# Kernel optimization log

Hardware: AMD Instinct MI355X
Metric: run time of the kernel (lower is better)

Reference implementation:

```python
import jax, jax.numpy as jnp
import numpy as np
from jax import lax

B, NQ, C = 2, 1024, 2048
H, DH = 16, 128
G, CD = 4, 512          # off_grps, off_dim = C // G
LR, HR = 24, 72         # low-res grid side, high-res grid side
INTER = 64
K = LR * LR             # sampled K/V tokens (grid_size == lr_size)


def setup_inputs() -> dict:
    key = jax.random.key(0)
    ks = jax.random.split(key, 16)
    s = 0.02
    d = {}
    d['hidden_states'] = jax.random.normal(ks[0], (B, NQ, C), jnp.float32)
    d['image_hd'] = jax.random.normal(ks[1], (B, HR * HR, C), jnp.float32)
    d['wq'] = jax.random.normal(ks[2], (C, C), jnp.float32) * s
    d['wk'] = jax.random.normal(ks[3], (C, C), jnp.float32) * s
    d['wv'] = jax.random.normal(ks[4], (C, C), jnp.float32) * s
    d['wo'] = jax.random.normal(ks[5], (C, C), jnp.float32) * s
    d['conv_dw_w'] = jax.random.normal(ks[6], (CD, 1, 3, 3), jnp.float32) * s
    d['ln1_w'] = jnp.ones((CD,), jnp.float32)
    d['ln1_b'] = jnp.zeros((CD,), jnp.float32)
    d['conv_lr_proj_w'] = jax.random.normal(ks[7], (INTER, CD), jnp.float32) * s
    d['proj_int_w'] = jax.random.normal(ks[8], (INTER, CD), jnp.float32) * s
    d['proj_int_b'] = jnp.zeros((INTER,), jnp.float32)
    d['ln2_w'] = jnp.ones((INTER,), jnp.float32)
    d['ln2_b'] = jnp.zeros((INTER,), jnp.float32)
    d['conv_off_w'] = jax.random.normal(ks[9], (2, INTER), jnp.float32) * s
    d['k_hd_w'] = jax.random.normal(ks[10], (C, C), jnp.float32) * s
    d['k_hd_b'] = jnp.zeros((C,), jnp.float32)
    d['v_hd_w'] = jax.random.normal(ks[11], (C, C), jnp.float32) * s
    d['v_hd_b'] = jnp.zeros((C,), jnp.float32)
    return d


def _ln_channels(x, w, b, eps=1e-5):
    # LayerNorm2d: normalize over channel axis of [N, C, H, W]
    mu = jnp.mean(x, axis=1, keepdims=True)
    var = jnp.var(x, axis=1, keepdims=True)
    xn = (x - mu) * lax.rsqrt(var + eps)
    return xn * w[None, :, None, None] + b[None, :, None, None]


def _tokens_to_grid(x, S):
    # [B, S*S, C] -> [B*G, CD, S, S]  (group channels like einops '(b) (h w) (g c) -> (b g) c h w')
    return x.reshape(B, S, S, G, CD).transpose(0, 3, 4, 1, 2).reshape(B * G, CD, S, S)


def _bilinear_sample(img, grid):
    # img [N, C, Hh, Wh]; grid [N, K, 2] (x, y) normalized to [-1, 1], align_corners=True
    N, Cc, Hh, Wh = img.shape
    x = (grid[..., 0] + 1.0) * 0.5 * (Wh - 1)
    y = (grid[..., 1] + 1.0) * 0.5 * (Hh - 1)
    x0f, y0f = jnp.floor(x), jnp.floor(y)
    wx = (x - x0f)[:, None, :]
    wy = (y - y0f)[:, None, :]
    x0 = jnp.clip(x0f.astype(jnp.int32), 0, Wh - 1)
    x1 = jnp.clip(x0 + 1, 0, Wh - 1)
    y0 = jnp.clip(y0f.astype(jnp.int32), 0, Hh - 1)
    y1 = jnp.clip(y0 + 1, 0, Hh - 1)
    imgf = img.reshape(N, Cc, Hh * Wh)
    gather = jax.vmap(lambda im, ix: im[:, ix])  # ([C,HW],[K]) -> [C,K]
    v00 = gather(imgf, y0 * Wh + x0)
    v01 = gather(imgf, y0 * Wh + x1)
    v10 = gather(imgf, y1 * Wh + x0)
    v11 = gather(imgf, y1 * Wh + x1)
    return (v00 * (1 - wx) * (1 - wy) + v01 * wx * (1 - wy)
            + v10 * (1 - wx) * wy + v11 * wx * wy)  # [N, C, K]


def _ref_grid():
    # normalized reference points as in _grid_generate (centers / (S-1) * 2 - 1)
    yy = (jnp.linspace(0.5, LR - 0.5, LR) / (LR - 1.0)) * 2.0 - 1.0
    xx = (jnp.linspace(0.5, LR - 0.5, LR) / (LR - 1.0)) * 2.0 - 1.0
    gy, gx = jnp.meshgrid(yy, xx, indexing='ij')
    return jnp.stack([gx, gy], axis=-1).reshape(K, 2)  # (x, y)


def reference(hidden_states, image_hd, wq, wk, wv, wo, conv_dw_w, ln1_w, ln1_b,
              conv_lr_proj_w, proj_int_w, proj_int_b, ln2_w, ln2_b, conv_off_w,
              k_hd_w, k_hd_b, v_hd_w, v_hd_b):
    # ---- QKV on the full sequence ----
    q = hidden_states @ wq.T
    k_txt = hidden_states @ wk.T
    v_txt = hidden_states @ wv.T

    # ---- offset network on LR image tokens (first LR*LR tokens) ----
    lr = _tokens_to_grid(hidden_states[:, :K, :], LR)          # [B*G, CD, LR, LR]
    x = lax.conv_general_dilated(lr, conv_dw_w, (1, 1), 'SAME',
                                 feature_group_count=CD,
                                 dimension_numbers=('NCHW', 'OIHW', 'NCHW'))
    x = jax.nn.silu(x)
    x = _ln_channels(x, ln1_w, ln1_b)
    x = jnp.einsum('nchw,oc->nohw', x, conv_lr_proj_w)          # 1x1 conv -> [B*G, INTER, LR, LR]
    # intention gate from spatially pooled group features
    pooled = jnp.mean(lr, axis=(2, 3))                          # [B*G, CD]
    gate = jax.nn.sigmoid(pooled @ proj_int_w.T + proj_int_b)   # [B*G, INTER]
    x = x * gate[:, :, None, None]
    x = _ln_channels(x, ln2_w, ln2_b)
    off = jnp.einsum('nchw,oc->nohw', x, conv_off_w)            # [B*G, 2, LR, LR]
    off = off.transpose(0, 2, 3, 1).reshape(B * G, K, 2)        # (x, y)
    pos = jnp.tanh(_ref_grid()[None] + off)                     # sampling locs in [-1, 1]

    # ---- deformable gather from HD features ----
    hd = _tokens_to_grid(image_hd, HR)                          # [B*G, CD, HR, HR]
    samp = _bilinear_sample(hd, pos)                            # [B*G, CD, K]
    samp = samp.reshape(B, G, CD, K).transpose(0, 3, 1, 2).reshape(B, K, C)
    k_hd = samp @ k_hd_w.T + k_hd_b
    v_hd = samp @ v_hd_w.T + v_hd_b

    # ---- attention: causal over text tokens, HD tokens fully visible ----
    k_all = jnp.concatenate([k_txt, k_hd], axis=1)              # [B, NQ+K, C]
    v_all = jnp.concatenate([v_txt, v_hd], axis=1)
    qh = q.reshape(B, NQ, H, DH).transpose(0, 2, 1, 3)
    kh = k_all.reshape(B, NQ + K, H, DH).transpose(0, 2, 1, 3)
    vh = v_all.reshape(B, NQ + K, H, DH).transpose(0, 2, 1, 3)
    scores = jnp.einsum('bhqd,bhkd->bhqk', qh, kh) / jnp.sqrt(jnp.float32(DH))
    col = jnp.arange(NQ + K)
    row = jnp.arange(NQ)
    allow = (col[None, :] >= NQ) | (col[None, :] <= row[:, None])
    scores = jnp.where(allow[None, None], scores, jnp.float32(-1e9))
    attn = jax.nn.softmax(scores, axis=-1)
    out = jnp.einsum('bhqk,bhkd->bhqd', attn, vh)
    out = out.transpose(0, 2, 1, 3).reshape(B, NQ, C)
    return out @ wo.T
```

## Files before the change

kernel.cpp:

```cpp
#include <hip/hip_runtime.h>

typedef unsigned short u16;
typedef unsigned int u32;
typedef __attribute__((ext_vector_type(8))) short bf8;
typedef __attribute__((ext_vector_type(4))) float f4;
typedef __attribute__((ext_vector_type(4))) unsigned short us4;

constexpr int B = 2;
constexpr int NQ = 1024;
constexpr int C = 2048;
constexpr int DH = 128;
constexpr int G = 4;
constexpr int CD = 512;
constexpr int LR = 24;
constexpr int HR = 72;
constexpr int INTER = 64;
constexpr int K = LR * LR;
constexpr int NKV = NQ + K;

#define MFMA16(a, b, c) __builtin_amdgcn_mfma_f32_16x16x32_bf16(a, b, c, 0, 0, 0)
#define GLDS(g, l)                                                         \
  __builtin_amdgcn_global_load_lds(                                        \
      (const __attribute__((address_space(1))) void*)(g),                  \
      (__attribute__((address_space(3))) void*)(l), 16, 0, 0)
#define SB()                               \
  do {                                     \
    __builtin_amdgcn_sched_barrier(0);     \
    __builtin_amdgcn_s_barrier();          \
    __builtin_amdgcn_sched_barrier(0);     \
  } while (0)
#define WVM(n)                                              \
  do {                                                      \
    asm volatile("s_waitcnt vmcnt(" #n ")" ::: "memory");   \
    __builtin_amdgcn_sched_barrier(0);                      \
  } while (0)

__device__ __forceinline__ u16 f2bf1(float f) {
  u32 u = __float_as_uint(f);
  u32 r = (u + 0x7fffu + ((u >> 16) & 1u)) >> 16;
  return (u16)r;
}

__global__ __launch_bounds__(256) void f2bf_k9(
    const float* __restrict__ s0, const float* __restrict__ s1,
    const float* __restrict__ s2, const float* __restrict__ s3,
    const float* __restrict__ s4, const float* __restrict__ s5,
    const float* __restrict__ s6, const float* __restrict__ plrw,
    const float* __restrict__ cdw, u16* __restrict__ d0, u16* __restrict__ d1,
    u16* __restrict__ d2, u16* __restrict__ d3, u16* __restrict__ d4,
    u16* __restrict__ d5, u16* __restrict__ d6, float* __restrict__ wt,
    float* __restrict__ x1, float* __restrict__ pooled) {
  __shared__ float SH[32 * 577];
  const int y = blockIdx.y;
  const int t = threadIdx.x;
  if (y == 7) {
    if (blockIdx.x >= 128) return;
    const int idx = blockIdx.x * 256 + t;
    wt[idx] = plrw[(idx & 63) * 512 + (idx >> 6)];
    return;
  }
  if (y == 8) {
    if (blockIdx.x >= 128) return;
    const int n = blockIdx.x >> 4, cg = blockIdx.x & 15;
    const int b = n >> 2, g = n & 3;
    const int c0 = cg * 32;
    {
      const int c = t & 31, pr = t >> 5;
      const float* src = s0 + (size_t)b * 1024 * 2048 + g * 512 + c0 + c;
#pragma unroll 4
      for (int j = 0; j < 72; ++j) {
        const int p = j * 8 + pr;
        SH[c * 577 + p] = src[(size_t)p * 2048];
      }
    }
    __syncthreads();
    {
      const int c = t >> 3, seg = t & 7;
      float s = 0.f;
      for (int i = 0; i < 72; ++i) s += SH[c * 577 + seg * 72 + i];
      s += __shfl_xor(s, 1);
      s += __shfl_xor(s, 2);
      s += __shfl_xor(s, 4);
      if (seg == 0) pooled[n * 512 + c0 + c] = s * (1.f / 576.f);
    }
    const size_t base_out = (size_t)(n * 512 + c0) * 576;
    for (int j = 0; j < 72; ++j) {
      const int idx = j * 256 + t;
      const int c = idx / 576, p = idx - c * 576;
      const int yy0 = p / 24, xx0 = p - yy0 * 24;
      const float* wp = cdw + (c0 + c) * 9;
      float s = 0.f;
#pragma unroll
      for (int dy = -1; dy <= 1; ++dy)
#pragma unroll
        for (int dx = -1; dx <= 1; ++dx) {
          const int yy = yy0 + dy, xx = xx0 + dx;
          if (yy < 0 || yy >= 24 || xx < 0 || xx >= 24) continue;
          s += SH[c * 577 + yy * 24 + xx] * wp[(dy + 1) * 3 + dx + 1];
        }
      x1[base_out + idx] = s / (1.f + expf(-s));
    }
    return;
  }
  const float* s;
  u16* d;
  switch (y) {
    case 0: s = s0; d = d0; break;
    case 1: s = s1; d = d1; break;
    case 2: s = s2; d = d2; break;
    case 3: s = s3; d = d3; break;
    case 4: s = s4; d = d4; break;
    case 5: s = s5; d = d5; break;
    default: s = s6; d = d6; break;
  }
  u16* L = (u16*)SH;
  const int pc = blockIdx.x;
  const int mb = pc >> 5, kb = pc & 31;
  const int rin = t >> 2, c0 = (t & 3) * 16;
  const float* src = s + (size_t)(mb * 64 + rin) * 2048 + kb * 64 + c0;
#pragma unroll
  for (int j = 0; j < 16; j += 4) {
    float4 v = *(const float4*)(src + j);
    L[rin * 68 + c0 + j] = f2bf1(v.x);
    L[rin * 68 + c0 + j + 1] = f2bf1(v.y);
    L[rin * 68 + c0 + j + 2] = f2bf1(v.z);
    L[rin * 68 + c0 + j + 3] = f2bf1(v.w);
  }
  __syncthreads();
  u16* dst = d + (size_t)pc * 4096 + t * 16;
#pragma unroll
  for (int gg = 0; gg < 2; ++gg) {
    const int g = t * 2 + gg;
    const int rh = g & 15, ks2 = (g >> 4) & 3, kc = (g >> 6) & 1, fr = g >> 7;
    const int row = fr * 16 + rh, cc = kc * 32 + ks2 * 8;
    us4 o0, o1;
    o0.x = L[row * 68 + cc];     o0.y = L[row * 68 + cc + 1];
    o0.z = L[row * 68 + cc + 2]; o0.w = L[row * 68 + cc + 3];
    o1.x = L[row * 68 + cc + 4]; o1.y = L[row * 68 + cc + 5];
    o1.z = L[row * 68 + cc + 6]; o1.w = L[row * 68 + cc + 7];
    *(us4*)(dst + gg * 8) = o0;
    *(us4*)(dst + gg * 8 + 4) = o1;
  }
}

__global__ __launch_bounds__(512, 2) void gemm256(
    const u16* __restrict__ Ast, const u16* __restrict__ Wq,
    const u16* __restrict__ Wk, const u16* __restrict__ Wv,
    u16* __restrict__ outq, u16* __restrict__ kg, u16* __restrict__ vg) {
  __shared__ u16 As[2][4][4096];
  __shared__ u16 Bs[2][4][4096];
  const int tid = threadIdx.x, lane = tid & 63, w = tid >> 6;
  const int ks = lane >> 4, r = lane & 15;
  const int bid = blockIdx.x;
  const int wm = w >> 2, wn = w & 3;
  const int swz = (bid & 7) * 24 + (bid >> 3);
  const int mt = swz / 24, nt = swz % 24;
  const u16* Wst = (nt < 8) ? Wq : (nt < 16) ? Wk : Wv;
  const int nb0 = (nt & 7) * 4;
  const int mb0 = mt * 4;

#define ST_A03(bi, kt)                                                        \
  do {                                                                        \
    GLDS(Ast + ((size_t)(mb0 + 0) * 32 + (kt)) * 4096 + tid * 8,              \
         &As[bi][0][tid * 8]);                                                \
    GLDS(Ast + ((size_t)(mb0 + 2) * 32 + (kt)) * 4096 + tid * 8,              \
         &As[bi][2][tid * 8]);                                                \
  } while (0)
#define ST_A47(bi, kt)                                                        \
  do {                                                                        \
    GLDS(Ast + ((size_t)(mb0 + 1) * 32 + (kt)) * 4096 + tid * 8,              \
         &As[bi][1][tid * 8]);                                                \
    GLDS(Ast + ((size_t)(mb0 + 3) * 32 + (kt)) * 4096 + tid * 8,              \
         &As[bi][3][tid * 8]);                                                \
  } while (0)
#define ST_B01(bi, kt)                                                        \
  do {                                                                        \
    GLDS(Wst + ((size_t)(nb0 + 0) * 32 + (kt)) * 4096 + tid * 8,              \
         &Bs[bi][0][tid * 8]);                                                \
    GLDS(Wst + ((size_t)(nb0 + 1) * 32 + (kt)) * 4096 + tid * 8,              \
         &Bs[bi][1][tid * 8]);                                                \
  } while (0)
#define ST_B23(bi, kt)                                                        \
  do {                                                                        \
    GLDS(Wst + ((size_t)(nb0 + 2) * 32 + (kt)) * 4096 + tid * 8,              \
         &Bs[bi][2][tid * 8]);                                                \
    GLDS(Wst + ((size_t)(nb0 + 3) * 32 + (kt)) * 4096 + tid * 8,              \
         &Bs[bi][3][tid * 8]);                                                \
  } while (0)
#define RD_A(dst, bi, half, kc)                                               \
  _Pragma("unroll") for (int i2 = 0; i2 < 4; ++i2) dst[i2] =                  \
      *(const bf8*)(&As[bi][wm * 2 + (half)]                                  \
                       [((i2 * 2 + (kc)) * 4 + ks) * 128 + r * 8]);
#define RD_B(dst, bi, kc)                                                     \
  _Pragma("unroll") for (int j2 = 0; j2 < 4; ++j2) dst[j2] =                  \
      *(const bf8*)(&Bs[bi][wn][((j2 * 2 + (kc)) * 4 + ks) * 128 + r * 8]);
#define MM(ACC, AF, BF)                                                       \
  do {                                                                        \
    __builtin_amdgcn_s_setprio(1);                                            \
    _Pragma("unroll") for (int i3 = 0; i3 < 4; ++i3)                          \
        _Pragma("unroll") for (int j3 = 0; j3 < 4; ++j3) ACC[i3][j3] =        \
            MFMA16(AF[i3], BF[j3], ACC[i3][j3]);                              \
    __builtin_amdgcn_s_setprio(0);                                            \
  } while (0)

  f4 accA[4][4], accB[4][4];
#pragma unroll
  for (int i = 0; i < 4; ++i)
#pragma unroll
    for (int j = 0; j < 4; ++j) {
      accA[i][j] = f4{0.f, 0.f, 0.f, 0.f};
      accB[i][j] = f4{0.f, 0.f, 0.f, 0.f};
    }
  bf8 af[4], b0[4], b1[4];

  ST_A03(0, 0); ST_B01(0, 0); ST_B23(0, 0); ST_A47(0, 0);
  ST_A03(1, 1); ST_B01(1, 1);
  WVM(6);
  SB();

  for (int t = 0; t < 32; ++t) {
    const int buf = t & 1;
    RD_A(af, buf, 0, 0);
    RD_B(b0, buf, 0);
    if (t + 1 < 32) ST_B23(buf ^ 1, t + 1);
    SB();
    MM(accA, af, b0);
    SB();
    RD_A(af, buf, 0, 1);
    RD_B(b1, buf, 1);
    if (t + 1 < 32) ST_A47(buf ^ 1, t + 1);
    SB();
    MM(accA, af, b1);
    if (t + 1 < 32) { WVM(8); } else { WVM(0); }
    SB();
    RD_A(af, buf, 1, 0);
    if (t + 2 < 32) ST_A03(buf, t + 2);
    SB();
    MM(accB, af, b0);
    SB();
    RD_A(af, buf, 1, 1);
    if (t + 2 < 32) ST_B01(buf, t + 2);
    SB();
    MM(accB, af, b1);
    if (t + 2 < 32) { WVM(6); } else if (t + 1 < 32) { WVM(2); }
    SB();
  }

#define EPI(ACC, HALF)                                                        \
  _Pragma("unroll") for (int i = 0; i < 4; ++i)                               \
      _Pragma("unroll") for (int j = 0; j < 4; ++j)                           \
          _Pragma("unroll") for (int rr = 0; rr < 4; ++rr) {                  \
    const int m = mt * 256 + wm * 128 + (HALF)*64 + i * 16 + ks * 4 + rr;     \
    const int n = nt * 256 + wn * 64 + j * 16 + r;                            \
    const float v = ACC[i][j][rr];                                            \
    const int sel = n >> 11, nn = n & 2047, hh = nn >> 7, dd = nn & 127;      \
    const int bb = m >> 10, qq = m & 1023;                                    \
    const u16 bv = f2bf1(v);                                                  \
    if (sel == 0) {                                                           \
      outq[(size_t)m * 2048 + nn] = bv;                                       \
    } else if (sel == 1) {                                                    \
      kg[(((size_t)(bb * 16 + hh) * 50 + (qq >> 5)) * 16 + (dd >> 3)) * 256 + \
         (qq & 31) * 8 + (dd & 7)] = bv;                                      \
    } else {                                                                  \
      vg[((size_t)(bb * 16 + hh) * 200 + (qq >> 3)) * 1024 + dd * 8 +         \
         (qq & 7)] = bv;                                                      \
    }                                                                         \
  }
  EPI(accA, 0)
  EPI(accB, 1)
#undef EPI
}

template <int MODE>
__global__ __launch_bounds__(256) void gemm_ho(
    const u16* __restrict__ Ast, const u16* __restrict__ W0,
    const u16* __restrict__ W1, const float* __restrict__ khb,
    const float* __restrict__ vhb, u16* __restrict__ kg,
    u16* __restrict__ vg, float* __restrict__ outf) {
  __shared__ u16 As[3][4096];
  __shared__ u16 Bs[3][4096];
  const int tid = threadIdx.x, lane = tid & 63, w = tid >> 6;
  const int wr = w >> 1, wc = w & 1;
  const int ksl = lane >> 4, rl = lane & 15;
  int mt, nt;
  const u16* Wp;
  if (MODE == 0) {
    const int xcd = blockIdx.x & 7, idx = blockIdx.x >> 3;
    mt = idx >> 2;
    nt = xcd * 4 + (idx & 3);
    Wp = (nt < 16) ? W0 : W1;
  } else {
    const int xcd = blockIdx.x & 7, idx = blockIdx.x >> 3;
    mt = (xcd >> 2) * 8 + idx / 4;
    nt = (xcd & 3) * 4 + idx % 4;
    Wp = W0;
  }
  const int ma0 = mt * 2;
  const int nb0 = (nt & 15) * 2;

#define GST2(dstArr, srcBase, tb0, kt)                                     \
  do {                                                                     \
    const int kb_ = (kt) >> 1, kc_ = (kt) & 1;                             \
    _Pragma("unroll") for (int r2 = 0; r2 < 2; ++r2) {                     \
      const int run = r2 * 4 + w;                                          \
      GLDS(srcBase + ((size_t)((tb0) + (run >> 2)) * 32 + kb_) * 4096 +    \
               (run & 3) * 1024 + kc_ * 512 + lane * 8,                    \
           &dstArr[run * 512 + lane * 8]);                                 \
    }                                                                      \
  } while (0)

  f4 acc[4][4];
#pragma unroll
  for (int i = 0; i < 4; ++i)
#pragma unroll
    for (int j = 0; j < 4; ++j) acc[i][j] = f4{0.f, 0.f, 0.f, 0.f};

  GST2(As[0], Ast, ma0, 0);
  GST2(Bs[0], Wp, nb0, 0);
  GST2(As[1], Ast, ma0, 1);
  GST2(Bs[1], Wp, nb0, 1);
  int rd = 0;
  for (int kt = 0; kt < 64; ++kt) {
    SB();
    if (kt + 2 < 64) {
      const int wb = (rd + 2 >= 3) ? rd - 1 : rd + 2;
      GST2(As[wb], Ast, ma0, kt + 2);
      GST2(Bs[wb], Wp, nb0, kt + 2);
      WVM(8);
    } else if (kt + 1 < 64) {
      WVM(4);
    } else {
      WVM(0);
    }
    SB();
    bf8 af[4], bw[4];
#pragma unroll
    for (int i = 0; i < 4; ++i)
      af[i] = *(const bf8*)(&As[rd][(wr * 4 + i) * 512 + ksl * 128 + rl * 8]);
#pragma unroll
    for (int j = 0; j < 4; ++j)
      bw[j] = *(const bf8*)(&Bs[rd][(wc * 4 + j) * 512 + ksl * 128 + rl * 8]);
    __builtin_amdgcn_s_setprio(1);
#pragma unroll
    for (int i = 0; i < 4; ++i)
#pragma unroll
      for (int j = 0; j < 4; ++j)
        acc[i][j] = MFMA16(af[i], bw[j], acc[i][j]);
    __builtin_amdgcn_s_setprio(0);
    rd = (rd + 1 >= 3) ? 0 : rd + 1;
  }
#undef GST2

  const int rbase = ksl * 4;
  if (MODE == 1) {
#pragma unroll
    for (int i = 0; i < 4; ++i)
#pragma unroll
      for (int j = 0; j < 4; ++j) {
        const int n = nt * 128 + wc * 64 + j * 16 + rl;
#pragma unroll
        for (int rr = 0; rr < 4; ++rr) {
          const int m = mt * 128 + wr * 64 + i * 16 + rbase + rr;
          outf[(size_t)m * 2048 + n] = acc[i][j][rr];
        }
      }
  } else {
    const bool is_v = (nt >= 16);
    const float* bias = is_v ? vhb : khb;
#pragma unroll
    for (int i = 0; i < 4; ++i)
#pragma unroll
      for (int j = 0; j < 4; ++j) {
        const int nn = (nt & 15) * 128 + wc * 64 + j * 16 + rl;
        const int hh = nn >> 7, dd = nn & 127;
#pragma unroll
        for (int rr = 0; rr < 4; ++rr) {
          const int m = mt * 128 + wr * 64 + i * 16 + rbase + rr;
          const int bb = m / 576;
          const int kv = 1024 + (m - bb * 576);
          const u16 bv = f2bf1(acc[i][j][rr] + bias[nn]);
          if (!is_v) {
            kg[(((size_t)(bb * 16 + hh) * 50 + (kv >> 5)) * 16 + (dd >> 3)) *
                   256 +
               (kv & 31) * 8 + (dd & 7)] = bv;
          } else {
            vg[((size_t)(bb * 16 + hh) * 200 + (kv >> 3)) * 1024 + dd * 8 +
               (kv & 7)] = bv;
          }
        }
      }
  }
}

__global__ __launch_bounds__(256) void lnproj_gate(
    const float* __restrict__ x1, const float* __restrict__ ln1w,
    const float* __restrict__ ln1b, const float* __restrict__ wt,
    const float* __restrict__ pooled, const float* __restrict__ piw,
    const float* __restrict__ pib, float* __restrict__ x2,
    float* __restrict__ gate) {
  __shared__ float Xs[512][68];
  __shared__ float rs[4][64], rss[4][64];
  const int bidx = blockIdx.x;
  const int t = threadIdx.x;
  if (bidx >= 72) {
    const int idx = (bidx - 72) * 256 + t;
    const int n = idx >> 6, o = idx & 63;
    const float* pb = pooled + n * 512;
    const float* wb = piw + o * 512;
    float s = pib[o];
    for (int c = 0; c < 512; ++c) s += pb[c] * wb[c];
    gate[idx] = 1.f / (1.f + expf(-s));
    return;
  }
  const int n = bidx / 9, pc = bidx % 9;
  const int p0 = pc * 64;
  {
    const int pl = t & 63, c4 = t >> 6;
    const float* src = x1 + (size_t)n * 512 * 576 + p0 + pl;
#pragma unroll 4
    for (int j = 0; j < 128; ++j) {
      const int c = j * 4 + c4;
      Xs[c][pl] = src[(size_t)c * 576];
    }
  }
  __syncthreads();
  {
    const int pl = t & 63, q = t >> 6;
    float s = 0.f, ss = 0.f;
    for (int c = q * 128; c < q * 128 + 128; ++c) {
      const float v = Xs[c][pl];
      s += v;
      ss += v * v;
    }
    rs[q][pl] = s;
    rss[q][pl] = ss;
    __syncthreads();
    const float S = rs[0][pl] + rs[1][pl] + rs[2][pl] + rs[3][pl];
    const float SS = rss[0][pl] + rss[1][pl] + rss[2][pl] + rss[3][pl];
    const float mean = S * (1.f / 512.f);
    const float inv = rsqrtf(SS * (1.f / 512.f) - mean * mean + 1e-5f);
    for (int c = q * 128; c < q * 128 + 128; ++c)
      Xs[c][pl] = (Xs[c][pl] - mean) * inv * ln1w[c] + ln1b[c];
  }
  __syncthreads();
  {
    const int o4 = (t & 15) * 4, pl0 = (t >> 4) * 4;
    float acc[4][4] = {};
    for (int c = 0; c < 512; ++c) {
      const f4 xv = *(const f4*)(&Xs[c][pl0]);
      const f4 wv = *(const f4*)(&wt[c * 64 + o4]);
#pragma unroll
      for (int i = 0; i < 4; ++i)
#pragma unroll
        for (int j = 0; j < 4; ++j) acc[i][j] += wv[i] * xv[j];
    }
#pragma unroll
    for (int i = 0; i < 4; ++i) {
      f4 ov;
      ov[0] = acc[i][0]; ov[1] = acc[i][1];
      ov[2] = acc[i][2]; ov[3] = acc[i][3];
      *(f4*)(&x2[(size_t)(n * 64 + o4 + i) * 576 + p0 + pl0]) = ov;
    }
  }
}

__global__ __launch_bounds__(256) void pos_sample(
    const float* __restrict__ x2, const float* __restrict__ gate,
    const float* __restrict__ ln2w, const float* __restrict__ ln2b,
    const float* __restrict__ offw, const float* __restrict__ img,
    u16* __restrict__ sampst) {
  const int bk = blockIdx.x;
  const int b = bk / K, k = bk % K;
  __shared__ int s_idx[G][4];
  __shared__ float s_w[G][4];
  const int t = threadIdx.x;
  const int g = t >> 6, lane = t & 63;
  {
    const int n = b * G + g;
    float v = x2[((size_t)n * INTER + lane) * K + k] * gate[n * INTER + lane];
    float s = v, ss = v * v;
    for (int o = 32; o; o >>= 1) {
      s += __shfl_xor(s, o);
      ss += __shfl_xor(ss, o);
    }
    const float mean = s * (1.f / INTER);
    const float var = ss * (1.f / INTER) - mean * mean;
    const float xn = (v - mean) * rsqrtf(var + 1e-5f) * ln2w[lane] + ln2b[lane];
    float ox = xn * offw[lane];
    float oy = xn * offw[INTER + lane];
    for (int o = 32; o; o >>= 1) {
      ox += __shfl_xor(ox, o);
      oy += __shfl_xor(oy, o);
    }
    if (lane == 0) {
      const int yi = k / LR, xi = k % LR;
      const float rx = (xi + 0.5f) / 23.f * 2.f - 1.f;
      const float ry = (yi + 0.5f) / 23.f * 2.f - 1.f;
      const float px = tanhf(rx + ox), py = tanhf(ry + oy);
      const float x = (px + 1.f) * 0.5f * (HR - 1);
      const float y = (py + 1.f) * 0.5f * (HR - 1);
      const float x0f = floorf(x), y0f = floorf(y);
      const float wx = x - x0f, wy = y - y0f;
      const int x0 = min(max((int)x0f, 0), HR - 1);
      const int x1 = min(x0 + 1, HR - 1);
      const int y0 = min(max((int)y0f, 0), HR - 1);
      const int y1 = min(y0 + 1, HR - 1);
      s_idx[g][0] = y0 * HR + x0;
      s_idx[g][1] = y0 * HR + x1;
      s_idx[g][2] = y1 * HR + x0;
      s_idx[g][3] = y1 * HR + x1;
      s_w[g][0] = (1.f - wx) * (1.f - wy);
      s_w[g][1] = wx * (1.f - wy);
      s_w[g][2] = (1.f - wx) * wy;
      s_w[g][3] = wx * wy;
    }
  }
  __syncthreads();
  const int m = b * 576 + k;
  const int mb = m >> 6, fr = (m >> 4) & 3, r = m & 15;
  const int ch0 = t * 8;
  const int gg = ch0 >> 9;
  const float* ib = img + (size_t)b * HR * HR * C + ch0;
  float v[8];
#pragma unroll
  for (int j = 0; j < 8; ++j) v[j] = 0.f;
#pragma unroll
  for (int q = 0; q < 4; ++q) {
    const float wq_ = s_w[gg][q];
    const float* p = ib + (size_t)s_idx[gg][q] * C;
    const float4 a = *(const float4*)p;
    const float4 c = *(const float4*)(p + 4);
    v[0] += wq_ * a.x; v[1] += wq_ * a.y; v[2] += wq_ * a.z; v[3] += wq_ * a.w;
    v[4] += wq_ * c.x; v[5] += wq_ * c.y; v[6] += wq_ * c.z; v[7] += wq_ * c.w;
  }
  const int kb = ch0 >> 6, kc = (ch0 >> 5) & 1, ks3 = (ch0 >> 3) & 3;
  u16* dst = sampst + ((size_t)(mb * 32 + kb)) * 4096 +
             (((fr * 2 + kc) * 4 + ks3) * 16 + r) * 8;
  us4 o0, o1;
  o0.x = f2bf1(v[0]); o0.y = f2bf1(v[1]); o0.z = f2bf1(v[2]); o0.w = f2bf1(v[3]);
  o1.x = f2bf1(v[4]); o1.y = f2bf1(v[5]); o1.z = f2bf1(v[6]); o1.w = f2bf1(v[7]);
  *(us4*)dst = o0;
  *(us4*)(dst + 4) = o1;
}

__global__ __launch_bounds__(256) void attn_u(
    const u16* __restrict__ qb, const u16* __restrict__ kg,
    const u16* __restrict__ vg, u16* __restrict__ aob_st) {
  const int i = blockIdx.x;
  const int pair = i & 255, half = i >> 8;
  const int bh = pair & 31;
  const int q8 = pair >> 5;
  const int qblk = half ? (15 - q8) : q8;
  const int b = bh >> 4, h = bh & 15;
  const int q0 = qblk * 64;
  const int tid = threadIdx.x, lane = tid & 63, w = tid >> 6;
  const int qw = q0 + w * 16;
  const int col = lane & 15, kpart = lane >> 4, rbase = kpart * 4;
  __shared__ u16 Ks[2][4096];
  __shared__ u16 Vs[2][4096];
  __shared__ u16 Pl[4][16 * 40];
  bf8 qf[4];
  {
    const u16* qp =
        qb + (size_t)(b * 1024 + qw + col) * 2048 + h * 128 + kpart * 8;
#pragma unroll
    for (int dc = 0; dc < 4; ++dc) qf[dc] = *(const bf8*)(qp + dc * 32);
  }
  f4 o[8];
#pragma unroll
  for (int df = 0; df < 8; ++df) o[df] = f4{0.f, 0.f, 0.f, 0.f};
  float m_r[4] = {-1e30f, -1e30f, -1e30f, -1e30f};
  float l_p[4] = {0.f, 0.f, 0.f, 0.f};
  const float scale = 0.08838834764831845f;
  const int nt_text = (q0 + 64) >> 5;
  const int nt = nt_text + 18;
  const u16* kbh = kg + (size_t)bh * (NKV * 128);
  const u16* vbh = vg + (size_t)bh * (NKV * 128);
  u16* pw = &Pl[w][0];

#define ASTAGE(bi, kv0)                                                       \
  do {                                                                        \
    const u16* gk = kbh + (size_t)((kv0) >> 5) * 4096 + w * 1024 + lane * 8;  \
    GLDS(gk, &Ks[bi][w * 1024 + lane * 8]);                                   \
    GLDS(gk + 512, &Ks[bi][w * 1024 + 512 + lane * 8]);                       \
    const u16* gv = vbh + (size_t)((kv0) >> 3) * 1024 + w * 1024 + lane * 8;  \
    GLDS(gv, &Vs[bi][w * 1024 + lane * 8]);                                   \
    GLDS(gv + 512, &Vs[bi][w * 1024 + 512 + lane * 8]);                       \
  } while (0)

  ASTAGE(0, 0);
  int cur = 0;
  for (int t = 0; t < nt; ++t) {
    const bool is_text = t < nt_text;
    const int kv0 = is_text ? (t << 5) : (1024 + ((t - nt_text) << 5));
    SB();
    if (t + 1 < nt) {
      const int t1 = t + 1;
      const int kv1 =
          (t1 < nt_text) ? (t1 << 5) : (1024 + ((t1 - nt_text) << 5));
      ASTAGE(cur ^ 1, kv1);
      WVM(4);
    } else {
      WVM(0);
    }
    SB();
    const u16* ksb = &Ks[cur][0];
    const u16* vsb = &Vs[cur][0];
    f4 s0 = {0.f, 0.f, 0.f, 0.f}, s1 = {0.f, 0.f, 0.f, 0.f};
    __builtin_amdgcn_s_setprio(1);
#pragma unroll
    for (int dc = 0; dc < 4; ++dc) {
      const int dblk = dc * 4 + kpart;
      bf8 k0f = *(const bf8*)(ksb + (dblk * 32 + col) * 8);
      bf8 k1f = *(const bf8*)(ksb + (dblk * 32 + 16 + col) * 8);
      s0 = MFMA16(qf[dc], k0f, s0);
      s1 = MFMA16(qf[dc], k1f, s1);
    }
    __builtin_amdgcn_s_setprio(0);
    float sa[4], sc[4], loc[4], p0[4], p1[4];
    bool grow = false;
    const bool need_mask = is_text && (kv0 + 31 > qw);
#pragma unroll
    for (int rr = 0; rr < 4; ++rr) {
      float a = s0[rr] * scale, c2 = s1[rr] * scale;
      if (need_mask) {
        const int qg = qw + rbase + rr;
        if (kv0 + col > qg) a = -1e30f;
        if (kv0 + 16 + col > qg) c2 = -1e30f;
      }
      sa[rr] = a; sc[rr] = c2;
      loc[rr] = fmaxf(a, c2);
      grow |= (loc[rr] > m_r[rr] + 8.f);
    }
    if (__any(grow)) {
      float fr[4];
#pragma unroll
      for (int rr = 0; rr < 4; ++rr) {
        float mx = loc[rr];
        mx = fmaxf(mx, __shfl_xor(mx, 1));
        mx = fmaxf(mx, __shfl_xor(mx, 2));
        mx = fmaxf(mx, __shfl_xor(mx, 4));
        mx = fmaxf(mx, __shfl_xor(mx, 8));
        const float mn = fmaxf(m_r[rr], mx);
        fr[rr] = __expf(m_r[rr] - mn);
        m_r[rr] = mn;
        p0[rr] = __expf(sa[rr] - mn);
        p1[rr] = __expf(sc[rr] - mn);
        l_p[rr] = l_p[rr] * fr[rr] + p0[rr] + p1[rr];
      }
#pragma unroll
      for (int df = 0; df < 8; ++df) {
        o[df][0] *= fr[0]; o[df][1] *= fr[1];
        o[df][2] *= fr[2]; o[df][3] *= fr[3];
      }
    } else {
#pragma unroll
      for (int rr = 0; rr < 4; ++rr) {
        p0[rr] = __expf(sa[rr] - m_r[rr]);
        p1[rr] = __expf(sc[rr] - m_r[rr]);
        l_p[rr] += p0[rr] + p1[rr];
      }
    }
#pragma unroll
    for (int rr = 0; rr < 4; ++rr) {
      pw[(rbase + rr) * 40 + col] = f2bf1(p0[rr]);
      pw[(rbase + rr) * 40 + 16 + col] = f2bf1(p1[rr]);
    }
    bf8 pa = *(const bf8*)(pw + col * 40 + kpart * 8);
    __builtin_amdgcn_s_setprio(1);
#pragma unroll
    for (int df = 0; df < 8; ++df) {
      bf8 vf = *(const bf8*)(vsb + (kpart * 128 + df * 16 + col) * 8);
      o[df] = MFMA16(pa, vf, o[df]);
    }
    __builtin_amdgcn_s_setprio(0);
    cur ^= 1;
  }
#undef ASTAGE
  float inv[4];
#pragma unroll
  for (int rr = 0; rr < 4; ++rr) {
    float ps = l_p[rr];
    ps += __shfl_xor(ps, 1);
    ps += __shfl_xor(ps, 2);
    ps += __shfl_xor(ps, 4);
    ps += __shfl_xor(ps, 8);
    inv[rr] = 1.f / ps;
  }
#pragma unroll
  for (int rr = 0; rr < 4; ++rr) {
    const int m = b * 1024 + qw + rbase + rr;
    const int mb = m >> 6, fr3 = (m >> 4) & 3, r16 = m & 15;
#pragma unroll
    for (int df = 0; df < 8; ++df) {
      const int ncol = h * 128 + df * 16 + col;
      const int kb = ncol >> 6, kc = (ncol >> 5) & 1, ks3 = (ncol >> 3) & 3,
                j0 = ncol & 7;
      aob_st[((size_t)(mb * 32 + kb)) * 4096 +
             (((fr3 * 2 + kc) * 4 + ks3) * 16 + r16) * 8 + j0] =
          f2bf1(o[df][rr] * inv[rr]);
    }
  }
}

extern "C" void kernel_launch(void* const* d_in, const int* in_sizes, int n_in,
                              void* d_out, int out_size, void* d_ws,
                              size_t ws_size, hipStream_t stream) {
  const float* hs = (const float*)d_in[0];
  const float* img = (const float*)d_in[1];
  const float* wq = (const float*)d_in[2];
  const float* wk = (const float*)d_in[3];
  const float* wv = (const float*)d_in[4];
  const float* wo = (const float*)d_in[5];
  const float* cdw = (const float*)d_in[6];
  const float* ln1w = (const float*)d_in[7];
  const float* ln1b = (const float*)d_in[8];
  const float* plrw = (const float*)d_in[9];
  const float* piw = (const float*)d_in[10];
  const float* pib = (const float*)d_in[11];
  const float* ln2w = (const float*)d_in[12];
  const float* ln2b = (const float*)d_in[13];
  const float* offw = (const float*)d_in[14];
  const float* khw = (const float*)d_in[15];
  const float* khb = (const float*)d_in[16];
  const float* vhw = (const float*)d_in[17];
  const float* vhb = (const float*)d_in[18];
  float* outp = (float*)d_out;

  u16* wsp = (u16*)d_ws;
  const size_t SZ = 4194304;
  u16* hs_st = wsp;
  u16* wq_st = wsp + SZ;
  u16* wk_st = wsp + 2 * SZ;
  u16* wv_st = wsp + 3 * SZ;
  u16* wo_st = wsp + 4 * SZ;
  u16* khw_st = wsp + 5 * SZ;
  u16* vhw_st = wsp + 6 * SZ;
  u16* qb_bf = wsp + 7 * SZ;
  u16* samp_st = wsp + 8 * SZ;
  u16* kg = wsp + 8 * SZ + 2359296;
  u16* vg = kg + 6553600;
  float* x1b = (float*)kg + 2359296;
  float* x2b = x1b + 2359296;
  float* poolb = x2b + 294912;
  float* gb = poolb + 4096;
  float* wtb = (float*)(vg + 6553600);
  u16* aob_st = wq_st;

  dim3 blk(256);
  f2bf_k9<<<dim3(1024, 9), blk, 0, stream>>>(
      hs, wq, wk, wv, wo, khw, vhw, plrw, cdw, hs_st, wq_st, wk_st, wv_st,
      wo_st, khw_st, vhw_st, wtb, x1b, poolb);
  lnproj_gate<<<dim3(74), blk, 0, stream>>>(x1b, ln1w, ln1b, wtb, poolb, piw,
                                            pib, x2b, gb);
  pos_sample<<<dim3(B * K), blk, 0, stream>>>(x2b, gb, ln2w, ln2b, offw, img,
                                              samp_st);
  gemm256<<<dim3(192), dim3(512), 0, stream>>>(hs_st, wq_st, wk_st, wv_st,
                                               qb_bf, kg, vg);
  gemm_ho<0><<<dim3(288), blk, 0, stream>>>(samp_st, khw_st, vhw_st, khb, vhb,
                                            kg, vg, nullptr);
  attn_u<<<dim3(512), blk, 0, stream>>>(qb_bf, kg, vg, aob_st);
  gemm_ho<1><<<dim3(256), blk, 0, stream>>>(aob_st, wo_st, nullptr, nullptr,
                                            nullptr, nullptr, nullptr, outp);
}
```

Measured before the change: 374.4 us.

## Fuse HD K/V projection GEMM into QKV GEMM launch and split conv blocks finer

Merges the separate high-res K/V projection GEMM into the QKV GEMM kernel as extra blocks (192 QKV blocks plus 144 HD blocks, each HD block computing both K and V tiles using 8 waves), removing one launch and letting the two GEMMs run concurrently to fill the GPU. The output projection becomes a dedicated non-templated kernel. The depthwise-conv/pooling part of the prep kernel also uses 16-channel blocks instead of 32 to double parallelism and halve shared memory. The HD path shares A tiles across K and V but runs inside a 512-thread, high-LDS kernel, which may limit occupancy or imbalance the block tail.

```diff
diff --git a/kernel.cpp b/kernel.cpp
--- a/kernel.cpp
+++ b/kernel.cpp
@@ -41,7 +41,7 @@
   return (u16)r;
 }
 
-__global__ __launch_bounds__(256) void f2bf_k9(
+__global__ __launch_bounds__(256) void f2bf_k9b(
     const float* __restrict__ s0, const float* __restrict__ s1,
     const float* __restrict__ s2, const float* __restrict__ s3,
     const float* __restrict__ s4, const float* __restrict__ s5,
@@ -50,7 +50,7 @@
     u16* __restrict__ d2, u16* __restrict__ d3, u16* __restrict__ d4,
     u16* __restrict__ d5, u16* __restrict__ d6, float* __restrict__ wt,
     float* __restrict__ x1, float* __restrict__ pooled) {
-  __shared__ float SH[32 * 577];
+  __shared__ float SH[16 * 577];
   const int y = blockIdx.y;
   const int t = threadIdx.x;
   if (y == 7) {
@@ -60,31 +60,32 @@
     return;
   }
   if (y == 8) {
-    if (blockIdx.x >= 128) return;
-    const int n = blockIdx.x >> 4, cg = blockIdx.x & 15;
+    if (blockIdx.x >= 256) return;
+    const int n = blockIdx.x >> 5, cg = blockIdx.x & 31;
     const int b = n >> 2, g = n & 3;
-    const int c0 = cg * 32;
+    const int c0 = cg * 16;
     {
-      const int c = t & 31, pr = t >> 5;
+      const int c = t & 15, pr = t >> 4;
       const float* src = s0 + (size_t)b * 1024 * 2048 + g * 512 + c0 + c;
 #pragma unroll 4
-      for (int j = 0; j < 72; ++j) {
-        const int p = j * 8 + pr;
+      for (int j = 0; j < 36; ++j) {
+        const int p = j * 16 + pr;
         SH[c * 577 + p] = src[(size_t)p * 2048];
       }
     }
     __syncthreads();
     {
-      const int c = t >> 3, seg = t & 7;
+      const int c = t >> 4, seg = t & 15;
       float s = 0.f;
-      for (int i = 0; i < 72; ++i) s += SH[c * 577 + seg * 72 + i];
+      for (int i = 0; i < 36; ++i) s += SH[c * 577 + seg * 36 + i];
       s += __shfl_xor(s, 1);
       s += __shfl_xor(s, 2);
       s += __shfl_xor(s, 4);
+      s += __shfl_xor(s, 8);
       if (seg == 0) pooled[n * 512 + c0 + c] = s * (1.f / 576.f);
     }
     const size_t base_out = (size_t)(n * 512 + c0) * 576;
-    for (int j = 0; j < 72; ++j) {
+    for (int j = 0; j < 36; ++j) {
       const int idx = j * 256 + t;
       const int c = idx / 576, p = idx - c * 576;
       const int yy0 = p / 24, xx0 = p - yy0 * 24;
@@ -143,21 +144,26 @@
   }
 }
 
-__global__ __launch_bounds__(512, 2) void gemm256(
+__global__ __launch_bounds__(512, 2) void gemm_qkv_hd(
     const u16* __restrict__ Ast, const u16* __restrict__ Wq,
     const u16* __restrict__ Wk, const u16* __restrict__ Wv,
-    u16* __restrict__ outq, u16* __restrict__ kg, u16* __restrict__ vg) {
+    const u16* __restrict__ sampst, const u16* __restrict__ khwst,
+    const u16* __restrict__ vhwst, const float* __restrict__ khb,
+    const float* __restrict__ vhb, u16* __restrict__ outq,
+    u16* __restrict__ kg, u16* __restrict__ vg) {
   __shared__ u16 As[2][4][4096];
   __shared__ u16 Bs[2][4][4096];
   const int tid = threadIdx.x, lane = tid & 63, w = tid >> 6;
   const int ks = lane >> 4, r = lane & 15;
   const int bid = blockIdx.x;
-  const int wm = w >> 2, wn = w & 3;
-  const int swz = (bid & 7) * 24 + (bid >> 3);
-  const int mt = swz / 24, nt = swz % 24;
-  const u16* Wst = (nt < 8) ? Wq : (nt < 16) ? Wk : Wv;
-  const int nb0 = (nt & 7) * 4;
-  const int mb0 = mt * 4;
+
+  if (bid < 192) {
+    const int wm = w >> 2, wn = w & 3;
+    const int swz = (bid & 7) * 24 + (bid >> 3);
+    const int mt = swz / 24, nt = swz % 24;
+    const u16* Wst = (nt < 8) ? Wq : (nt < 16) ? Wk : Wv;
+    const int nb0 = (nt & 7) * 4;
+    const int mb0 = mt * 4;
 
 #define ST_A03(bi, kt)                                                        \
   do {                                                                        \
@@ -203,48 +209,48 @@
     __builtin_amdgcn_s_setprio(0);                                            \
   } while (0)
 
-  f4 accA[4][4], accB[4][4];
-#pragma unroll
-  for (int i = 0; i < 4; ++i)
-#pragma unroll
-    for (int j = 0; j < 4; ++j) {
-      accA[i][j] = f4{0.f, 0.f, 0.f, 0.f};
-      accB[i][j] = f4{0.f, 0.f, 0.f, 0.f};
-    }
-  bf8 af[4], b0[4], b1[4];
-
-  ST_A03(0, 0); ST_B01(0, 0); ST_B23(0, 0); ST_A47(0, 0);
-  ST_A03(1, 1); ST_B01(1, 1);
-  WVM(6);
-  SB();
-
-  for (int t = 0; t < 32; ++t) {
-    const int buf = t & 1;
-    RD_A(af, buf, 0, 0);
-    RD_B(b0, buf, 0);
-    if (t + 1 < 32) ST_B23(buf ^ 1, t + 1);
+    f4 accA[4][4], accB[4][4];
+#pragma unroll
+    for (int i = 0; i < 4; ++i)
+#pragma unroll
+      for (int j = 0; j < 4; ++j) {
+        accA[i][j] = f4{0.f, 0.f, 0.f, 0.f};
+        accB[i][j] = f4{0.f, 0.f, 0.f, 0.f};
+      }
+    bf8 af[4], b0[4], b1[4];
+
+    ST_A03(0, 0); ST_B01(0, 0); ST_B23(0, 0); ST_A47(0, 0);
+    ST_A03(1, 1); ST_B01(1, 1);
+    WVM(6);
     SB();
-    MM(accA, af, b0);
-    SB();
-    RD_A(af, buf, 0, 1);
-    RD_B(b1, buf, 1);
-    if (t + 1 < 32) ST_A47(buf ^ 1, t + 1);
-    SB();
-    MM(accA, af, b1);
-    if (t + 1 < 32) { WVM(8); } else { WVM(0); }
-    SB();
-    RD_A(af, buf, 1, 0);
-    if (t + 2 < 32) ST_A03(buf, t + 2);
-    SB();
-    MM(accB, af, b0);
-    SB();
-    RD_A(af, buf, 1, 1);
-    if (t + 2 < 32) ST_B01(buf, t + 2);
-    SB();
-    MM(accB, af, b1);
-    if (t + 2 < 32) { WVM(6); } else if (t + 1 < 32) { WVM(2); }
-    SB();
-  }
+
+    for (int t = 0; t < 32; ++t) {
+      const int buf = t & 1;
+      RD_A(af, buf, 0, 0);
+      RD_B(b0, buf, 0);
+      if (t + 1 < 32) ST_B23(buf ^ 1, t + 1);
+      SB();
+      MM(accA, af, b0);
+      SB();
+      RD_A(af, buf, 0, 1);
+      RD_B(b1, buf, 1);
+      if (t + 1 < 32) ST_A47(buf ^ 1, t + 1);
+      SB();
+      MM(accA, af, b1);
+      if (t + 1 < 32) { WVM(8); } else { WVM(0); }
+      SB();
+      RD_A(af, buf, 1, 0);
+      if (t + 2 < 32) ST_A03(buf, t + 2);
+      SB();
+      MM(accB, af, b0);
+      SB();
+      RD_A(af, buf, 1, 1);
+      if (t + 2 < 32) ST_B01(buf, t + 2);
+      SB();
+      MM(accB, af, b1);
+      if (t + 2 < 32) { WVM(6); } else if (t + 1 < 32) { WVM(2); }
+      SB();
+    }
 
 #define EPI(ACC, HALF)                                                        \
   _Pragma("unroll") for (int i = 0; i < 4; ++i)                               \
@@ -266,37 +272,118 @@
          (qq & 7)] = bv;                                                      \
     }                                                                         \
   }
-  EPI(accA, 0)
-  EPI(accB, 1)
+    EPI(accA, 0)
+    EPI(accB, 1)
 #undef EPI
+  } else {
+    u16* A3 = &As[0][0][0];
+    u16* Bk3 = &As[0][0][0] + 12288;
+    u16* Bv3 = &Bs[0][0][0];
+    const int hb = bid - 192;
+    const int mt = hb / 16, nt = hb % 16;
+    const int ma0 = mt * 2, nb0 = nt * 2;
+    const bool is_v = (w >= 4);
+    const int wv4 = w & 3;
+    const int wr = wv4 >> 1, wc = wv4 & 1;
+    const u16* Wsrc = is_v ? vhwst : khwst;
+    u16* Wdst = is_v ? Bv3 : Bk3;
+    const u16* Brd = is_v ? Bv3 : Bk3;
+
+#define HDST(bi, kt)                                                          \
+  do {                                                                        \
+    const int kb_ = (kt) >> 1, kc_ = (kt) & 1;                                \
+    GLDS(sampst + ((size_t)(ma0 + (w >> 2)) * 32 + kb_) * 4096 +              \
+             (w & 3) * 1024 + kc_ * 512 + lane * 8,                           \
+         &A3[(bi)*4096 + w * 512 + lane * 8]);                                \
+    _Pragma("unroll") for (int r2 = 0; r2 < 2; ++r2) {                        \
+      const int run = r2 * 4 + wv4;                                           \
+      GLDS(Wsrc + ((size_t)(nb0 + (run >> 2)) * 32 + kb_) * 4096 +            \
+               (run & 3) * 1024 + kc_ * 512 + lane * 8,                       \
+           &Wdst[(bi)*4096 + run * 512 + lane * 8]);                          \
+    }                                                                         \
+  } while (0)
+
+    f4 acc[4][4];
+#pragma unroll
+    for (int i = 0; i < 4; ++i)
+#pragma unroll
+      for (int j = 0; j < 4; ++j) acc[i][j] = f4{0.f, 0.f, 0.f, 0.f};
+
+    HDST(0, 0);
+    HDST(1, 1);
+    int rd = 0;
+    for (int kt = 0; kt < 64; ++kt) {
+      SB();
+      if (kt + 2 < 64) {
+        const int wb = (rd + 2 >= 3) ? rd - 1 : rd + 2;
+        HDST(wb, kt + 2);
+        WVM(6);
+      } else if (kt + 1 < 64) {
+        WVM(3);
+      } else {
+        WVM(0);
+      }
+      SB();
+      bf8 af2[4], bw[4];
+#pragma unroll
+      for (int i = 0; i < 4; ++i)
+        af2[i] =
+            *(const bf8*)(&A3[rd * 4096 + (wr * 4 + i) * 512 + ks * 128 + r * 8]);
+#pragma unroll
+      for (int j = 0; j < 4; ++j)
+        bw[j] =
+            *(const bf8*)(&Brd[rd * 4096 + (wc * 4 + j) * 512 + ks * 128 + r * 8]);
+      __builtin_amdgcn_s_setprio(1);
+#pragma unroll
+      for (int i = 0; i < 4; ++i)
+#pragma unroll
+        for (int j = 0; j < 4; ++j)
+          acc[i][j] = MFMA16(af2[i], bw[j], acc[i][j]);
+      __builtin_amdgcn_s_setprio(0);
+      rd = (rd + 1 >= 3) ? 0 : rd + 1;
+    }
+#undef HDST
+    const int rbase = ks * 4;
+    const float* bias = is_v ? vhb : khb;
+#pragma unroll
+    for (int i = 0; i < 4; ++i)
+#pragma unroll
+      for (int j = 0; j < 4; ++j) {
+        const int nn = nt * 128 + wc * 64 + j * 16 + r;
+        const int hh = nn >> 7, dd = nn & 127;
+#pragma unroll
+        for (int rr = 0; rr < 4; ++rr) {
+          const int m = mt * 128 + wr * 64 + i * 16 + rbase + rr;
+          const int bb = m / 576;
+          const int kv = 1024 + (m - bb * 576);
+          const u16 bv = f2bf1(acc[i][j][rr] + bias[nn]);
+          if (!is_v) {
+            kg[(((size_t)(bb * 16 + hh) * 50 + (kv >> 5)) * 16 + (dd >> 3)) *
+                   256 +
+               (kv & 31) * 8 + (dd & 7)] = bv;
+          } else {
+            vg[((size_t)(bb * 16 + hh) * 200 + (kv >> 3)) * 1024 + dd * 8 +
+               (kv & 7)] = bv;
+          }
+        }
+      }
+  }
 }
 
-template <int MODE>
-__global__ __launch_bounds__(256) void gemm_ho(
-    const u16* __restrict__ Ast, const u16* __restrict__ W0,
-    const u16* __restrict__ W1, const float* __restrict__ khb,
-    const float* __restrict__ vhb, u16* __restrict__ kg,
-    u16* __restrict__ vg, float* __restrict__ outf) {
+__global__ __launch_bounds__(256) void gemm_out3(const u16* __restrict__ Ast,
+                                                 const u16* __restrict__ W0,
+                                                 float* __restrict__ outf) {
   __shared__ u16 As[3][4096];
   __shared__ u16 Bs[3][4096];
   const int tid = threadIdx.x, lane = tid & 63, w = tid >> 6;
   const int wr = w >> 1, wc = w & 1;
   const int ksl = lane >> 4, rl = lane & 15;
-  int mt, nt;
-  const u16* Wp;
-  if (MODE == 0) {
-    const int xcd = blockIdx.x & 7, idx = blockIdx.x >> 3;
-    mt = idx >> 2;
-    nt = xcd * 4 + (idx & 3);
-    Wp = (nt < 16) ? W0 : W1;
-  } else {
-    const int xcd = blockIdx.x & 7, idx = blockIdx.x >> 3;
-    mt = (xcd >> 2) * 8 + idx / 4;
-    nt = (xcd & 3) * 4 + idx % 4;
-    Wp = W0;
-  }
+  const int xcd = blockIdx.x & 7, idx = blockIdx.x >> 3;
+  const int mt = (xcd >> 2) * 8 + idx / 4;
+  const int nt = (xcd & 3) * 4 + idx % 4;
+  const u16* Wp = W0;
   const int ma0 = mt * 2;
-  const int nb0 = (nt & 15) * 2;
+  const int nb0 = nt * 2;
 
 #define GST2(dstArr, srcBase, tb0, kt)                                     \
   do {                                                                     \
@@ -352,44 +439,17 @@
 #undef GST2
 
   const int rbase = ksl * 4;
-  if (MODE == 1) {
-#pragma unroll
-    for (int i = 0; i < 4; ++i)
-#pragma unroll
-      for (int j = 0; j < 4; ++j) {
-        const int n = nt * 128 + wc * 64 + j * 16 + rl;
-#pragma unroll
-        for (int rr = 0; rr < 4; ++rr) {
-          const int m = mt * 128 + wr * 64 + i * 16 + rbase + rr;
-          outf[(size_t)m * 2048 + n] = acc[i][j][rr];
-        }
+#pragma unroll
+  for (int i = 0; i < 4; ++i)
+#pragma unroll
+    for (int j = 0; j < 4; ++j) {
+      const int n = nt * 128 + wc * 64 + j * 16 + rl;
+#pragma unroll
+      for (int rr = 0; rr < 4; ++rr) {
+        const int m = mt * 128 + wr * 64 + i * 16 + rbase + rr;
+        outf[(size_t)m * 2048 + n] = acc[i][j][rr];
       }
-  } else {
-    const bool is_v = (nt >= 16);
-    const float* bias = is_v ? vhb : khb;
-#pragma unroll
-    for (int i = 0; i < 4; ++i)
-#pragma unroll
-      for (int j = 0; j < 4; ++j) {
-        const int nn = (nt & 15) * 128 + wc * 64 + j * 16 + rl;
-        const int hh = nn >> 7, dd = nn & 127;
-#pragma unroll
-        for (int rr = 0; rr < 4; ++rr) {
-          const int m = mt * 128 + wr * 64 + i * 16 + rbase + rr;
-          const int bb = m / 576;
-          const int kv = 1024 + (m - bb * 576);
-          const u16 bv = f2bf1(acc[i][j][rr] + bias[nn]);
-          if (!is_v) {
-            kg[(((size_t)(bb * 16 + hh) * 50 + (kv >> 5)) * 16 + (dd >> 3)) *
-                   256 +
-               (kv & 31) * 8 + (dd & 7)] = bv;
-          } else {
-            vg[((size_t)(bb * 16 + hh) * 200 + (kv >> 3)) * 1024 + dd * 8 +
-               (kv & 7)] = bv;
-          }
-        }
-      }
-  }
+    }
 }
 
 __global__ __launch_bounds__(256) void lnproj_gate(
@@ -748,18 +808,16 @@
   u16* aob_st = wq_st;
 
   dim3 blk(256);
-  f2bf_k9<<<dim3(1024, 9), blk, 0, stream>>>(
+  f2bf_k9b<<<dim3(1024, 9), blk, 0, stream>>>(
       hs, wq, wk, wv, wo, khw, vhw, plrw, cdw, hs_st, wq_st, wk_st, wv_st,
       wo_st, khw_st, vhw_st, wtb, x1b, poolb);
   lnproj_gate<<<dim3(74), blk, 0, stream>>>(x1b, ln1w, ln1b, wtb, poolb, piw,
                                             pib, x2b, gb);
   pos_sample<<<dim3(B * K), blk, 0, stream>>>(x2b, gb, ln2w, ln2b, offw, img,
                                               samp_st);
-  gemm256<<<dim3(192), dim3(512), 0, stream>>>(hs_st, wq_st, wk_st, wv_st,
-                                               qb_bf, kg, vg);
-  gemm_ho<0><<<dim3(288), blk, 0, stream>>>(samp_st, khw_st, vhw_st, khb, vhb,
-                                            kg, vg, nullptr);
+  gemm_qkv_hd<<<dim3(336), dim3(512), 0, stream>>>(
+      hs_st, wq_st, wk_st, wv_st, samp_st, khw_st, vhw_st, khb, vhb, qb_bf,
+      kg, vg);
   attn_u<<<dim3(512), blk, 0, stream>>>(qb_bf, kg, vg, aob_st);
-  gemm_ho<1><<<dim3(256), blk, 0, stream>>>(aob_st, wo_st, nullptr, nullptr,
-                                            nullptr, nullptr, nullptr, outp);
+  gemm_out3<<<dim3(256), blk, 0, stream>>>(aob_st, wo_st, outp);
 }
```

After: 338.0 us. 1.11x faster.
